# Kernel tuning notes

Hardware: AMD Instinct MI355X
Metric: run time of the kernel (lower is better)

## Reference

```python
import jax, jax.numpy as jnp
import numpy as np

G = 5            # semantic groups: head_spine, left_arm, right_arm, left_leg, right_leg
B = 131072       # batch of pose samples
K = 512          # tokens_per_group
D = 64           # token_dim
COMMITMENT_COST = 0.25


def setup_inputs() -> dict:
    key = jax.random.key(0)
    k1, k2 = jax.random.split(key)
    features = jax.random.normal(k1, (G, B, D), dtype=jnp.float32)
    # nn.Embedding init: uniform(-1/num_embeddings, 1/num_embeddings)
    codebooks = jax.random.uniform(k2, (G, K, D), dtype=jnp.float32,
                                   minval=-1.0 / K, maxval=1.0 / K)
    return {"features": features, "codebooks": codebooks}


def reference(features, codebooks):
    """features: [G, B, D], codebooks: [G, K, D].
    Returns (quantized [G,B,D], per_group_loss [G], total_loss scalar, indices [G,B]).
    """
    x_sq = jnp.sum(features ** 2, axis=-1, keepdims=True)          # [G, B, 1]
    e_sq = jnp.sum(codebooks ** 2, axis=-1)[:, None, :]            # [G, 1, K]
    cross = jnp.einsum('gbd,gkd->gbk', features, codebooks)        # [G, B, K]
    distances = x_sq + e_sq - 2.0 * cross

    indices = jnp.argmin(distances, axis=-1)                       # [G, B]
    # gather codebook rows (replaces one-hot scatter + matmul)
    quantized = jnp.take_along_axis(codebooks, indices[:, :, None], axis=1)  # [G, B, D]

    # per-group MSE losses (straight-through VQ loss)
    e_latent = jnp.mean((jax.lax.stop_gradient(quantized) - features) ** 2, axis=(1, 2))
    q_latent = jnp.mean((quantized - jax.lax.stop_gradient(features)) ** 2, axis=(1, 2))
    per_group_loss = q_latent + COMMITMENT_COST * e_latent          # [G]
    total_loss = jnp.sum(per_group_loss)

    # straight-through estimator
    quantized_st = features + jax.lax.stop_gradient(quantized - features)
    return quantized_st, per_group_loss, total_loss, indices
```

## Files before the change

kernel.cpp:

```cpp
#include <hip/hip_runtime.h>

typedef _Float16 half8 __attribute__((ext_vector_type(8)));
typedef float floatx16 __attribute__((ext_vector_type(16)));

constexpr int Gn = 5;
constexpr int Bn = 131072;
constexpr int Kn = 512;
constexpr int Dn = 64;

constexpr long long QOFF = (long long)Gn * Bn * Dn;
constexpr long long IOFF = QOFF + Gn + 1;
constexpr unsigned CAPE = 49152;

#define GLDS(gp, lp)  __builtin_amdgcn_global_load_lds( \
    (const __attribute__((address_space(1))) void*)(gp), \
    (__attribute__((address_space(3))) void*)(lp), 16, 0, 0)

__global__ void vq_prep(const float* __restrict__ code, float* __restrict__ esq,
                        _Float16* __restrict__ ch16, _Float16* __restrict__ esqt) {
    int i = blockIdx.x * blockDim.x + threadIdx.x;
    if (i >= Gn * Kn) return;
    const float4* c4 = reinterpret_cast<const float4*>(code + (long long)i * Dn);
    _Float16* hp = ch16 + (long long)i * Dn;
    float s0 = 0.f, s1 = 0.f, s2 = 0.f, s3 = 0.f;
#pragma unroll
    for (int j = 0; j < 16; ++j) {
        float4 v = c4[j];
        s0 += v.x * v.x; s1 += v.y * v.y; s2 += v.z * v.z; s3 += v.w * v.w;
        hp[4 * j + 0] = (_Float16)v.x;
        hp[4 * j + 1] = (_Float16)v.y;
        hp[4 * j + 2] = (_Float16)v.z;
        hp[4 * j + 3] = (_Float16)v.w;
    }
    float e = (s0 + s1) + (s2 + s3);
    esq[i] = e;
    int g = i >> 9, k = i & 511;
    esqt[(g << 9) + ((k & 31) << 4) + (k >> 5)] = (_Float16)(-(e * 1024.0f));
}

__global__ __launch_bounds__(256, 4) void vq_screen(
    const float* __restrict__ feat, const float* __restrict__ codef,
    const _Float16* __restrict__ ch16, const _Float16* __restrict__ esqt,
    float* __restrict__ out, float* __restrict__ accg,
    unsigned* __restrict__ cnt, unsigned* __restrict__ entries)
{
    __shared__ float4 smf[2 * 256];

    const int g = blockIdx.y;
    const int lane = threadIdx.x & 63;
    const int wv = threadIdx.x >> 6;
    const int l31 = lane & 31;
    const int hh = lane >> 5;
    const long long rowbase = (long long)blockIdx.x * 256 + wv * 64;
    const float MARGIN = 3.0e-5f;
    const int CLR = (int)0xFFFFFF00;

    half8 fH[2][4]; float xs[2];
#pragma unroll
    for (int t = 0; t < 2; ++t) {
        const float* rp = feat + ((long long)g * Bn + rowbase + t * 32 + l31) * Dn + hh * 8;
        float x = 0.f;
#pragma unroll
        for (int s = 0; s < 4; ++s) {
            float4 u0 = *(const float4*)(rp + 16 * s);
            float4 u1 = *(const float4*)(rp + 16 * s + 4);
            half8 h;
            h[0] = (_Float16)u0.x; h[1] = (_Float16)u0.y;
            h[2] = (_Float16)u0.z; h[3] = (_Float16)u0.w;
            h[4] = (_Float16)u1.x; h[5] = (_Float16)u1.y;
            h[6] = (_Float16)u1.z; h[7] = (_Float16)u1.w;
            fH[t][s] = h;
            x += u0.x*u0.x + u0.y*u0.y + u0.z*u0.z + u0.w*u0.w
               + u1.x*u1.x + u1.y*u1.y + u1.z*u1.z + u1.w*u1.w;
        }
        xs[t] = x + __shfl_xor(x, 32);
    }

    const half8* evp = (const half8*)(esqt + ((long long)g << 9) + l31 * 16);
    half8 ev0 = evp[0], ev1 = evp[1];

    half8 b5 = {(_Float16)0.f};
    b5[0] = hh ? (_Float16)0.f : (_Float16)4.8828125e-4f;

    const int cs = lane >> 3;
    const int u  = lane & 7;
    const int codeLocal = wv * 8 + cs;
    const float4* srcF4 = (const float4*)(ch16 + ((long long)g * Kn) * Dn);
    const float4* gsrc = srcF4 + codeLocal * 8 + (u ^ cs);
    const int rb0 = l31 * 8;
    const int rsw = l31 & 7;

    GLDS(gsrc, &smf[wv * 64]);
    __syncthreads();

    float v1[2] = {-3.0e38f, -3.0e38f}, v2[2] = {-3.0e38f, -3.0e38f};

#pragma unroll
    for (int ch = 0; ch < 16; ++ch) {
        const int buf = (ch & 1) * 256;
        if (ch + 1 < 16)
            GLDS(gsrc + (ch + 1) * 256, &smf[((ch + 1) & 1) * 256 + wv * 64]);

        half8 cH[4];
#pragma unroll
        for (int s = 0; s < 4; ++s)
            cH[s] = *(const half8*)&smf[buf + rb0 + ((hh + 2 * s) ^ rsw)];

        half8 a5 = {(_Float16)0.f};
        _Float16 eb = (ch < 8) ? ev0[ch] : ev1[ch - 8];
        a5[0] = hh ? (_Float16)0.f : eb;

        floatx16 acc0 = {0.f}, acc1 = {0.f};
#pragma unroll
        for (int s = 0; s < 4; ++s) {
            acc0 = __builtin_amdgcn_mfma_f32_32x32x16_f16(cH[s], fH[0][s], acc0, 0, 0, 0);
            acc1 = __builtin_amdgcn_mfma_f32_32x32x16_f16(cH[s], fH[1][s], acc1, 0, 0, 0);
        }
        acc0 = __builtin_amdgcn_mfma_f32_32x32x16_f16(a5, b5, acc0, 0, 0, 0);
        acc1 = __builtin_amdgcn_mfma_f32_32x32x16_f16(a5, b5, acc1, 0, 0, 0);

        const int idb = ch << 4;
#pragma unroll
        for (int r = 0; r < 16; ++r) {
            float c0 = __int_as_float((__float_as_int(acc0[r]) & CLR) | (idb | r));
            v2[0] = __builtin_amdgcn_fmed3f(v1[0], v2[0], c0);
            v1[0] = fmaxf(v1[0], c0);
            float c1 = __int_as_float((__float_as_int(acc1[r]) & CLR) | (idb | r));
            v2[1] = __builtin_amdgcn_fmed3f(v1[1], v2[1], c1);
            v1[1] = fmaxf(v1[1], c1);
        }
        __syncthreads();
    }

    int codew[2]; float v1c[2], v2c[2];
#pragma unroll
    for (int t = 0; t < 2; ++t) {
        float o1 = __shfl_xor(v1[t], 32);
        float o2 = __shfl_xor(v2[t], 32);
        float w1 = fmaxf(v1[t], o1);
        float w2 = fmaxf(fminf(v1[t], o1), fmaxf(v2[t], o2));
        int hsrc = (o1 > v1[t]) ? (hh ^ 1) : hh;
        int idw = __float_as_int(w1) & 255;
        int rr = idw & 15;
        codew[t] = ((idw >> 4) << 5) + (rr & 3) + 8 * (rr >> 2) + 4 * hsrc;
        v1c[t] = __int_as_float(__float_as_int(w1) & CLR);
        v2c[t] = __int_as_float(__float_as_int(w2) & CLR);
    }

#pragma unroll
    for (int t = 0; t < 2; ++t) {
        float* obase = out + ((long long)g * Bn + rowbase + t * 32) * Dn;
#pragma unroll
        for (int i = 0; i < 8; ++i) {
            int r = i * 4 + (lane >> 4);
            int c = __shfl(codew[t], r);
            float4 q = *(const float4*)(codef + ((long long)(g * Kn + c)) * Dn + (lane & 15) * 4);
            *(float4*)(obase + (long long)r * Dn + (lane & 15) * 4) = q;
        }
    }

    float lsum = 0.f;
    bool fl[2] = {false, false};
    unsigned rw[2] = {0u, 0u};
#pragma unroll
    for (int t = 0; t < 2; ++t) {
        if (hh == 0) {
            long long grow = rowbase + t * 32 + l31;
            out[IOFF + (long long)g * Bn + grow] = (float)codew[t];
            lsum += xs[t] - 2.0f * v1c[t];
            fl[t] = (v1c[t] - v2c[t] <= MARGIN);
            rw[t] = (unsigned)grow;
        }
    }

    unsigned long long m0 = __ballot(fl[0]);
    unsigned long long m1 = __ballot(fl[1]);
    unsigned tot = (unsigned)(__builtin_popcountll(m0) + __builtin_popcountll(m1));
    if (tot) {
        unsigned base = 0;
        if (lane == 0) base = atomicAdd(cnt, tot);
        base = (unsigned)__shfl((int)base, 0);
        unsigned long long lt = ((unsigned long long)1 << lane) - 1;
        if (fl[0]) {
            unsigned s = base + (unsigned)__builtin_popcountll(m0 & lt);
            if (s < CAPE) entries[s] = ((unsigned)g << 17) | rw[0];
        }
        if (fl[1]) {
            unsigned s = base + (unsigned)__builtin_popcountll(m0)
                              + (unsigned)__builtin_popcountll(m1 & lt);
            if (s < CAPE) entries[s] = ((unsigned)g << 17) | rw[1];
        }
    }
#pragma unroll
    for (int m = 1; m < 64; m <<= 1) lsum += __shfl_xor(lsum, m);
    if (lane == 0) atomicAdd(&accg[g], lsum);
}

__global__ __launch_bounds__(256) void vq_rescue(
    const float* __restrict__ feat, const float* __restrict__ codef,
    const float* __restrict__ esq, const unsigned* __restrict__ cnt,
    const unsigned* __restrict__ entries, float* __restrict__ out,
    const float* __restrict__ accg)
{
    if (blockIdx.x == 0 && threadIdx.x == 0) {
        float tot = 0.f;
#pragma unroll
        for (int g = 0; g < Gn; ++g) {
            float m = accg[g] / 8388608.0f;
            float l = m + 0.25f * m;
            out[QOFF + g] = l;
            tot += l;
        }
        out[QOFF + Gn] = tot;
    }

    const int lane = threadIdx.x & 63;
    const int wid = blockIdx.x * 4 + (threadIdx.x >> 6);
    const int nw = gridDim.x * 4;
    const int n = (int)min(*cnt, CAPE);

    for (int i = wid; i < n; i += nw) {
        unsigned e = entries[i];
        int g = e >> 17;
        long long b = e & 131071u;

        const float* xp = feat + ((long long)g * Bn + b) * Dn;
        float x[64];
#pragma unroll
        for (int j = 0; j < 16; ++j) {
            float4 u = ((const float4*)xp)[j];
            x[4*j] = u.x; x[4*j+1] = u.y; x[4*j+2] = u.z; x[4*j+3] = u.w;
        }
        float xsq;
        {
#pragma clang fp contract(off)
            float r0[8];
#pragma unroll
            for (int j = 0; j < 8; ++j) r0[j] = x[j] * x[j];
#pragma unroll
            for (int q = 8; q < 64; q += 8)
#pragma unroll
                for (int j = 0; j < 8; ++j) {
                    float s0 = x[q + j] * x[q + j];
                    r0[j] = r0[j] + s0;
                }
            xsq = ((r0[0] + r0[1]) + (r0[2] + r0[3])) + ((r0[4] + r0[5]) + (r0[6] + r0[7]));
        }

        const float* cg = codef + (long long)g * Kn * Dn;
        const float* eg = esq + g * Kn;
        float best = 3.4e38f; int bk = 0x7fffffff;
        for (int j = 0; j < 8; ++j) {
            int k = j * 64 + lane;
            const float4* cp = (const float4*)(cg + (long long)k * Dn);
            float d0 = 0.f, d1 = 0.f, d2 = 0.f, d3 = 0.f;
#pragma unroll
            for (int q = 0; q < 16; ++q) {
                float4 v = cp[q];
                d0 = fmaf(v.x, x[4*q+0], d0);
                d1 = fmaf(v.y, x[4*q+1], d1);
                d2 = fmaf(v.z, x[4*q+2], d2);
                d3 = fmaf(v.w, x[4*q+3], d3);
            }
            float dot = (d0 + d1) + (d2 + d3);
            float dist = (xsq + eg[k]) - 2.0f * dot;
            if (dist < best) { best = dist; bk = k; }
        }
#pragma unroll
        for (int m = 1; m < 64; m <<= 1) {
            float ov = __shfl_xor(best, m);
            int   ok = __shfl_xor(bk, m);
            if (ov < best || (ov == best && ok < bk)) { best = ov; bk = ok; }
        }
        if (lane == 0) out[IOFF + (long long)g * Bn + b] = (float)bk;
        out[((long long)g * Bn + b) * Dn + lane] = cg[(long long)bk * Dn + lane];
    }
}

extern "C" void kernel_launch(void* const* d_in, const int* in_sizes, int n_in,
                              void* d_out, int out_size, void* d_ws, size_t ws_size,
                              hipStream_t stream) {
    const float* feat = (const float*)d_in[0];
    const float* code = (const float*)d_in[1];
    float* out = (float*)d_out;

    char* w = (char*)d_ws;
    float*     acc     = (float*)w;
    unsigned*  cnt     = (unsigned*)(w + 64);
    float*     esq     = (float*)(w + 128);
    _Float16*  esqt    = (_Float16*)(w + 10368);
    _Float16*  ch16    = (_Float16*)(w + 15488);
    unsigned*  entries = (unsigned*)(w + 343168);

    hipMemsetAsync(w, 0, 128, stream);
    vq_prep<<<(Gn * Kn + 255) / 256, 256, 0, stream>>>(code, esq, ch16, esqt);
    dim3 grid(Bn / 256, Gn);
    vq_screen<<<grid, 256, 0, stream>>>(feat, code, ch16, esqt, out, acc, cnt, entries);
    vq_rescue<<<2048, 256, 0, stream>>>(feat, code, esq, cnt, entries, out, acc);
}
```

Baseline: 525.0 us.

## Batch four codebook chunks per barrier and split top-2 tracking chains

The codebook screening loop now stages four chunks per double-buffered LDS slot, so it runs 4 phases with 3 barriers instead of 16 chunks with a barrier each. The running top-2 max/median tracking is split into two independent chains per row tile, merged after the loop, to shorten the serial dependency of fmed3/fmax. This trades a 4x larger LDS footprint (32KB per block) for fewer syncs and more ILP, which may reduce occupancy.

```diff
diff --git a/kernel.cpp b/kernel.cpp
--- a/kernel.cpp
+++ b/kernel.cpp
@@ -44,7 +44,7 @@
     float* __restrict__ out, float* __restrict__ accg,
     unsigned* __restrict__ cnt, unsigned* __restrict__ entries)
 {
-    __shared__ float4 smf[2 * 256];
+    __shared__ float4 smf[2 * 1024];
 
     const int g = blockIdx.y;
     const int lane = threadIdx.x & 63;
@@ -90,56 +90,73 @@
     const int rb0 = l31 * 8;
     const int rsw = l31 & 7;
 
-    GLDS(gsrc, &smf[wv * 64]);
+#pragma unroll
+    for (int s4 = 0; s4 < 4; ++s4)
+        GLDS(gsrc + s4 * 256, &smf[s4 * 256 + wv * 64]);
     __syncthreads();
 
-    float v1[2] = {-3.0e38f, -3.0e38f}, v2[2] = {-3.0e38f, -3.0e38f};
-
-#pragma unroll
-    for (int ch = 0; ch < 16; ++ch) {
-        const int buf = (ch & 1) * 256;
-        if (ch + 1 < 16)
-            GLDS(gsrc + (ch + 1) * 256, &smf[((ch + 1) & 1) * 256 + wv * 64]);
-
-        half8 cH[4];
-#pragma unroll
-        for (int s = 0; s < 4; ++s)
-            cH[s] = *(const half8*)&smf[buf + rb0 + ((hh + 2 * s) ^ rsw)];
-
-        half8 a5 = {(_Float16)0.f};
-        _Float16 eb = (ch < 8) ? ev0[ch] : ev1[ch - 8];
-        a5[0] = hh ? (_Float16)0.f : eb;
-
-        floatx16 acc0 = {0.f}, acc1 = {0.f};
-#pragma unroll
-        for (int s = 0; s < 4; ++s) {
-            acc0 = __builtin_amdgcn_mfma_f32_32x32x16_f16(cH[s], fH[0][s], acc0, 0, 0, 0);
-            acc1 = __builtin_amdgcn_mfma_f32_32x32x16_f16(cH[s], fH[1][s], acc1, 0, 0, 0);
-        }
-        acc0 = __builtin_amdgcn_mfma_f32_32x32x16_f16(a5, b5, acc0, 0, 0, 0);
-        acc1 = __builtin_amdgcn_mfma_f32_32x32x16_f16(a5, b5, acc1, 0, 0, 0);
-
-        const int idb = ch << 4;
-#pragma unroll
-        for (int r = 0; r < 16; ++r) {
-            float c0 = __int_as_float((__float_as_int(acc0[r]) & CLR) | (idb | r));
-            v2[0] = __builtin_amdgcn_fmed3f(v1[0], v2[0], c0);
-            v1[0] = fmaxf(v1[0], c0);
-            float c1 = __int_as_float((__float_as_int(acc1[r]) & CLR) | (idb | r));
-            v2[1] = __builtin_amdgcn_fmed3f(v1[1], v2[1], c1);
-            v1[1] = fmaxf(v1[1], c1);
-        }
-        __syncthreads();
+    float v1h[2][2] = {{-3.0e38f, -3.0e38f}, {-3.0e38f, -3.0e38f}};
+    float v2h[2][2] = {{-3.0e38f, -3.0e38f}, {-3.0e38f, -3.0e38f}};
+
+#pragma unroll
+    for (int p = 0; p < 4; ++p) {
+        const int buf = (p & 1) * 1024;
+        if (p < 3) {
+#pragma unroll
+            for (int s4 = 0; s4 < 4; ++s4)
+                GLDS(gsrc + ((p + 1) * 4 + s4) * 256,
+                     &smf[((p + 1) & 1) * 1024 + s4 * 256 + wv * 64]);
+        }
+#pragma unroll
+        for (int s4 = 0; s4 < 4; ++s4) {
+            const int ch = p * 4 + s4;
+            const int cb = buf + s4 * 256;
+
+            half8 cH[4];
+#pragma unroll
+            for (int s = 0; s < 4; ++s)
+                cH[s] = *(const half8*)&smf[cb + rb0 + ((hh + 2 * s) ^ rsw)];
+
+            half8 a5 = {(_Float16)0.f};
+            _Float16 eb = (ch & 8) ? ev1[ch & 7] : ev0[ch & 7];
+            a5[0] = hh ? (_Float16)0.f : eb;
+
+            floatx16 acc0 = {0.f}, acc1 = {0.f};
+#pragma unroll
+            for (int s = 0; s < 4; ++s) {
+                acc0 = __builtin_amdgcn_mfma_f32_32x32x16_f16(cH[s], fH[0][s], acc0, 0, 0, 0);
+                acc1 = __builtin_amdgcn_mfma_f32_32x32x16_f16(cH[s], fH[1][s], acc1, 0, 0, 0);
+            }
+            acc0 = __builtin_amdgcn_mfma_f32_32x32x16_f16(a5, b5, acc0, 0, 0, 0);
+            acc1 = __builtin_amdgcn_mfma_f32_32x32x16_f16(a5, b5, acc1, 0, 0, 0);
+
+            const int idb = ch << 4;
+#pragma unroll
+            for (int r = 0; r < 16; ++r) {
+                const int hc = r >> 3;
+                float c0 = __int_as_float((__float_as_int(acc0[r]) & CLR) | (idb | r));
+                v2h[0][hc] = __builtin_amdgcn_fmed3f(v1h[0][hc], v2h[0][hc], c0);
+                v1h[0][hc] = fmaxf(v1h[0][hc], c0);
+                float c1 = __int_as_float((__float_as_int(acc1[r]) & CLR) | (idb | r));
+                v2h[1][hc] = __builtin_amdgcn_fmed3f(v1h[1][hc], v2h[1][hc], c1);
+                v1h[1][hc] = fmaxf(v1h[1][hc], c1);
+            }
+        }
+        if (p < 3) __syncthreads();
     }
 
     int codew[2]; float v1c[2], v2c[2];
 #pragma unroll
     for (int t = 0; t < 2; ++t) {
-        float o1 = __shfl_xor(v1[t], 32);
-        float o2 = __shfl_xor(v2[t], 32);
-        float w1 = fmaxf(v1[t], o1);
-        float w2 = fmaxf(fminf(v1[t], o1), fmaxf(v2[t], o2));
-        int hsrc = (o1 > v1[t]) ? (hh ^ 1) : hh;
+        float a1 = v1h[t][0], b1 = v1h[t][1];
+        float v1 = fmaxf(a1, b1);
+        float v2 = fmaxf(fminf(a1, b1), fmaxf(v2h[t][0], v2h[t][1]));
+
+        float o1 = __shfl_xor(v1, 32);
+        float o2 = __shfl_xor(v2, 32);
+        float w1 = fmaxf(v1, o1);
+        float w2 = fmaxf(fminf(v1, o1), fmaxf(v2, o2));
+        int hsrc = (o1 > v1) ? (hh ^ 1) : hh;
         int idw = __float_as_int(w1) & 255;
         int rr = idw & 15;
         codew[t] = ((idw >> 4) << 5) + (rr & 3) + 8 * (rr >> 2) + 4 * hsrc;
```

After: 525.4 us. No clear change (+0.1%).
